# Performance work log

Measured on AMD Instinct MI355X. Metric: run time of the kernel, lower is better.

Reference implementation:

```python
import jax, jax.numpy as jnp
import numpy as np

S = 128          # spatial grid size per axis
N = 100000       # active voxels
C_IN = 32
C_OUT = 32
FS = 3           # filter size per axis -> 27 offsets


def _build_rulebook():
    """Build submanifold-conv rulebook: for each active site and each of the
    27 filter offsets, the index of the active neighbor (or masked out)."""
    rng = np.random.default_rng(0)
    coords = rng.integers(0, S, size=(2 * N, 3))
    lin = coords[:, 0] * S * S + coords[:, 1] * S + coords[:, 2]
    lin = np.unique(lin)[:N]                      # sorted unique active sites
    xyz = np.stack([lin // (S * S), (lin // S) % S, lin % S], axis=1)  # [N,3]
    offs = np.stack(np.meshgrid(*([np.arange(FS) - FS // 2] * 3), indexing='ij'), -1).reshape(-1, 3)  # [27,3]
    nb = xyz[:, None, :] + offs[None, :, :]       # [N,27,3]
    inb = np.all((nb >= 0) & (nb < S), axis=-1)   # in-bounds
    nb_lin = nb[..., 0] * S * S + nb[..., 1] * S + nb[..., 2]
    pos = np.searchsorted(lin, nb_lin)
    pos_c = np.clip(pos, 0, N - 1)
    found = inb & (lin[pos_c] == nb_lin)
    nbr_idx = np.where(found, pos_c, 0).astype(np.int32)   # [N,27]
    return nbr_idx, found


def setup_inputs() -> dict:
    key = jax.random.key(0)
    k1, k2 = jax.random.split(key)
    nbr_idx, nbr_mask = _build_rulebook()
    K = FS ** 3
    std = (2.0 / C_IN / K) ** 0.5   # matches module init
    return {
        'features': jax.random.normal(k1, (N, C_IN), dtype=jnp.float32),
        'weight': std * jax.random.normal(k2, (K, C_IN, C_OUT), dtype=jnp.float32),
        'bias': jnp.zeros((C_OUT,), dtype=jnp.float32),
        'nbr_idx': jnp.asarray(nbr_idx),
        'nbr_mask': jnp.asarray(nbr_mask),
    }


def reference(features, weight, bias, nbr_idx, nbr_mask):
    # Submanifold sparse conv: gather active neighbors per filter offset,
    # multiply by per-offset [Cin,Cout] weight, accumulate at active sites.
    gathered = jnp.where(nbr_mask[:, :, None], features[nbr_idx], 0.0)  # [N,K,Cin]
    out = jnp.einsum('nki,kio->no', gathered, weight) + bias            # [N,Cout]
    return out
```

## Files before the change

kernel.cpp:

```cpp
#include <hip/hip_runtime.h>
#include <hip/hip_bf16.h>

#define NVOX 100000
#define CIN 32
#define COUT 32
#define KOFF 27
#define NTILE 6250

typedef __attribute__((ext_vector_type(8))) short short8;
typedef __attribute__((ext_vector_type(4))) float float4v;

__device__ __forceinline__ short f2bf(float x) {
    union { float f; unsigned u; } v; v.f = x;
    unsigned u = v.u;
    u += 0x7FFFu + ((u >> 16) & 1u);
    return (short)(u >> 16);
}

#define FEAT_BLOCKS 3126

__global__ __launch_bounds__(256) void cvt_kernel(
    const float* __restrict__ feat, const float* __restrict__ weight,
    unsigned short* __restrict__ fbf, short8* __restrict__ wfrag)
{
    if (blockIdx.x < FEAT_BLOCKS) {
        int i = (blockIdx.x * 256 + threadIdx.x) * 4;
        if (i < NVOX * CIN) {
            float4v f = *(const float4v*)(feat + i);
            short s[4] = { f2bf(f.x), f2bf(f.y), f2bf(f.z), f2bf(f.w) };
            *(ulonglong1*)(fbf + i) = *(ulonglong1*)s;
        } else if (i < (NVOX + 1) * CIN) {
            short s[4] = { 0, 0, 0, 0 };
            *(ulonglong1*)(fbf + i) = *(ulonglong1*)s;
        }
    } else {
        int g = (blockIdx.x - FEAT_BLOCKS) * 256 + threadIdx.x;
        if (g >= KOFF * 2 * 64) return;
        int k   = g >> 7;
        int rem = g & 127;
        int t   = rem >> 6;
        int ln  = rem & 63;
        int co  = t * 16 + (ln & 15);
        int cib = (ln >> 4) * 8;
        const float* wp = weight + (k * CIN + cib) * COUT + co;
        short8 b;
#pragma unroll
        for (int j = 0; j < 8; ++j) b[j] = f2bf(wp[j * COUT]);
        wfrag[g] = b;
    }
}

__global__ __launch_bounds__(512, 4) void subm_conv_kernel(
    const unsigned short* __restrict__ fbf,
    const short8* __restrict__ wfrag,
    const float* __restrict__ bias,
    const int* __restrict__ nbr_idx,
    const int* __restrict__ nbr_mask,
    float* __restrict__ out)
{
    __shared__ short8 wlds[KOFF * 2 * 64];

    const int tid  = threadIdx.x;
    const int lane = tid & 63;
    const int wave = tid >> 6;
    const int m    = lane & 15;
    const int quad = lane >> 4;
    const int tile = blockIdx.x * 8 + wave;
    const bool tv  = tile < NTILE;

    const int v0 = tile * 16;
    int v = v0 + m;
    if (v > NVOX - 1) v = NVOX - 1;
    const int base = v * KOFF;

    int enc[KOFF];
#pragma unroll
    for (int k = 0; k < KOFF; ++k) enc[k] = nbr_idx[base + k];
    int mok[KOFF];
#pragma unroll
    for (int k = 0; k < KOFF; ++k) mok[k] = nbr_mask[base + k];
#pragma unroll
    for (int k = 0; k < KOFF; ++k) enc[k] = (mok[k] ? enc[k] : NVOX) << 6;

    for (int g = tid; g < KOFF * 2 * 64; g += 512) wlds[g] = wfrag[g];
    __syncthreads();

    float4v acc0 = {0.f, 0.f, 0.f, 0.f};
    float4v acc1 = {0.f, 0.f, 0.f, 0.f};

    const char* fb   = (const char*)fbf;
    const int   boff = quad * 16;

    short8 abuf[8];
#pragma unroll
    for (int k = 0; k < 8; ++k)
        abuf[k] = *(const short8*)(fb + (size_t)(unsigned)enc[k] + boff);

#pragma unroll
    for (int k = 0; k < KOFF; ++k) {
        const int slot = k & 7;
        short8 a = abuf[slot];
        if (k + 8 < KOFF)
            abuf[slot] = *(const short8*)(fb + (size_t)(unsigned)enc[k + 8] + boff);

        short8 wb0 = wlds[k * 128 + lane];
        short8 wb1 = wlds[k * 128 + 64 + lane];
        acc0 = __builtin_amdgcn_mfma_f32_16x16x32_bf16(a, wb0, acc0, 0, 0, 0);
        acc1 = __builtin_amdgcn_mfma_f32_16x16x32_bf16(a, wb1, acc1, 0, 0, 0);
    }

    __syncthreads();
    float* tb = (float*)wlds + wave * (16 * 36);

    const float bs0 = bias[m];
    const float bs1 = bias[16 + m];
    if (tv) {
#pragma unroll
        for (int r = 0; r < 4; ++r) {
            tb[(quad * 4 + r) * 36 + m]      = acc0[r] + bs0;
            tb[(quad * 4 + r) * 36 + 16 + m] = acc1[r] + bs1;
        }
#pragma unroll
        for (int p = 0; p < 2; ++p) {
            int flat = p * 64 + lane;
            int row  = flat >> 3;
            int ch   = flat & 7;
            float4v val = *(const float4v*)(tb + row * 36 + ch * 4);
            *(float4v*)(out + (size_t)(v0 + row) * COUT + ch * 4) = val;
        }
    }
}

extern "C" void kernel_launch(void* const* d_in, const int* in_sizes, int n_in,
                              void* d_out, int out_size, void* d_ws, size_t ws_size,
                              hipStream_t stream) {
    const float* feat = (const float*)d_in[0];
    const float* wgt  = (const float*)d_in[1];
    const float* bias = (const float*)d_in[2];
    const int*   nidx = (const int*)d_in[3];
    const int*   nmsk = (const int*)d_in[4];
    float*       out  = (float*)d_out;

    char* ws = (char*)d_ws;
    unsigned short* fbf   = (unsigned short*)ws;
    short8*         wfrag = (short8*)(ws + 6400128);

    const int wgt_blocks = (KOFF * 2 * 64 + 255) / 256;
    cvt_kernel<<<FEAT_BLOCKS + wgt_blocks, 256, 0, stream>>>(feat, wgt, fbf, wfrag);

    const int block = 512;
    const int grid  = (NTILE + 7) / 8;
    subm_conv_kernel<<<grid, block, 0, stream>>>(fbf, wfrag, bias, nidx, nmsk, out);
}
```

Measured before the change: 99.82 us.

## Coalesce rulebook loads via LDS staging and skip all-empty filter offsets per wave

Each wave now loads its 16x27 neighbor index and mask block with contiguous int4 loads, stages the encoded offsets in LDS, and reads each row back as int4. This replaces the strided per-lane scalar loads. It also builds a wave-uniform bitmask of the offsets that have at least one active neighbor and skips the LDS weight reads and MFMAs for offsets with none. The cost is an extra barrier, LDS round-trips and branches inside the unrolled MFMA loop. With about 5% occupancy, many offsets may be empty across a whole 16-voxel tile.

```diff
diff --git a/kernel.cpp b/kernel.cpp
--- a/kernel.cpp
+++ b/kernel.cpp
@@ -6,9 +6,11 @@
 #define COUT 32
 #define KOFF 27
 #define NTILE 6250
+#define SENTE (NVOX << 6)
 
 typedef __attribute__((ext_vector_type(8))) short short8;
 typedef __attribute__((ext_vector_type(4))) float float4v;
+typedef __attribute__((ext_vector_type(4))) int   int4v;
 
 __device__ __forceinline__ short f2bf(float x) {
     union { float f; unsigned u; } v; v.f = x;
@@ -65,23 +67,51 @@
     const int wave = tid >> 6;
     const int m    = lane & 15;
     const int quad = lane >> 4;
-    const int tile = blockIdx.x * 8 + wave;
-    const bool tv  = tile < NTILE;
+    const int tile0 = blockIdx.x * 8 + wave;
+    const bool tv  = tile0 < NTILE;
+    const int tile = tv ? tile0 : (NTILE - 1);
+    const int v0   = tile * 16;
 
-    const int v0 = tile * 16;
-    int v = v0 + m;
-    if (v > NVOX - 1) v = NVOX - 1;
-    const int base = v * KOFF;
+    int* meta = (int*)wlds + wave * 448;
+    {
+        const int tb = v0 * KOFF;
+        const int j0 = lane * 4;
+        int4v ia = *(const int4v*)(nbr_idx  + tb + j0);
+        int4v ma = *(const int4v*)(nbr_mask + tb + j0);
+#pragma unroll
+        for (int c = 0; c < 4; ++c) {
+            int j = j0 + c;
+            meta[(j / 27) * 28 + (j % 27)] = (ma[c] ? ia[c] : NVOX) << 6;
+        }
+        if (j0 < 176) {
+            int4v ib = *(const int4v*)(nbr_idx  + tb + 256 + j0);
+            int4v mb = *(const int4v*)(nbr_mask + tb + 256 + j0);
+#pragma unroll
+            for (int c = 0; c < 4; ++c) {
+                int j = 256 + j0 + c;
+                meta[(j / 27) * 28 + (j % 27)] = (mb[c] ? ib[c] : NVOX) << 6;
+            }
+        }
+    }
 
-    int enc[KOFF];
+    int enc[28];
+    {
+        const int4v* mp = (const int4v*)(meta + m * 28);
 #pragma unroll
-    for (int k = 0; k < KOFF; ++k) enc[k] = nbr_idx[base + k];
-    int mok[KOFF];
+        for (int i = 0; i < 7; ++i) {
+            int4v t = mp[i];
+            enc[i * 4 + 0] = t.x; enc[i * 4 + 1] = t.y;
+            enc[i * 4 + 2] = t.z; enc[i * 4 + 3] = t.w;
+        }
+    }
+
+    unsigned bmv = 0;
 #pragma unroll
-    for (int k = 0; k < KOFF; ++k) mok[k] = nbr_mask[base + k];
-#pragma unroll
-    for (int k = 0; k < KOFF; ++k) enc[k] = (mok[k] ? enc[k] : NVOX) << 6;
+    for (int k = 0; k < KOFF; ++k)
+        bmv |= (__any(enc[k] != SENTE) ? 1u : 0u) << k;
+    const unsigned bm = (unsigned)__builtin_amdgcn_readfirstlane((int)bmv);
 
+    __syncthreads();
     for (int g = tid; g < KOFF * 2 * 64; g += 512) wlds[g] = wfrag[g];
     __syncthreads();
 
@@ -103,10 +133,12 @@
         if (k + 8 < KOFF)
             abuf[slot] = *(const short8*)(fb + (size_t)(unsigned)enc[k + 8] + boff);
 
-        short8 wb0 = wlds[k * 128 + lane];
-        short8 wb1 = wlds[k * 128 + 64 + lane];
-        acc0 = __builtin_amdgcn_mfma_f32_16x16x32_bf16(a, wb0, acc0, 0, 0, 0);
-        acc1 = __builtin_amdgcn_mfma_f32_16x16x32_bf16(a, wb1, acc1, 0, 0, 0);
+        if (bm & (1u << k)) {
+            short8 wb0 = wlds[k * 128 + lane];
+            short8 wb1 = wlds[k * 128 + 64 + lane];
+            acc0 = __builtin_amdgcn_mfma_f32_16x16x32_bf16(a, wb0, acc0, 0, 0, 0);
+            acc1 = __builtin_amdgcn_mfma_f32_16x16x32_bf16(a, wb1, acc1, 0, 0, 0);
+        }
     }
 
     __syncthreads();
```

After: 98.96 us. Within noise of the previous version (-0.9%).
